# Optimization experiments

Hardware: AMD Instinct MI355X
Metric: run time of the kernel (lower is better)

Reference implementation:

```python
import jax, jax.numpy as jnp
import numpy as np

IMG, P, CIN, D, K, L, H, FF, B = 512, 32, 3, 256, 8192, 6, 8, 1024, 32
GRID = IMG // P  # 16
DH = D // H
EPS = 1e-5


def _ln(x, w, b):
    m = x.mean(-1, keepdims=True)
    v = ((x - m) ** 2).mean(-1, keepdims=True)
    return (x - m) / jnp.sqrt(v + EPS) * w + b


def _mha(x, wqkv, bqkv, wo, bo):
    # x: (S, Bt, D) -- axis 0 is the attention axis (torch batch_first=False quirk)
    S, Bt, _ = x.shape
    qkv = x @ wqkv.T + bqkv
    q, k, v = jnp.split(qkv, 3, axis=-1)
    q = q.reshape(S, Bt, H, DH)
    k = k.reshape(S, Bt, H, DH)
    v = v.reshape(S, Bt, H, DH)
    scores = jnp.einsum('sbhd,tbhd->bhst', q, k) / jnp.sqrt(jnp.float32(DH))
    attn = jax.nn.softmax(scores, axis=-1)
    o = jnp.einsum('bhst,tbhd->sbhd', attn, v).reshape(S, Bt, D)
    return o @ wo.T + bo


def _conv_t(x, w, b, stride=2, pad=1):
    # w uses torch ConvTranspose2d layout (Cin, Cout, kH, kW)
    kH = w.shape[2]
    wf = jnp.flip(w, (2, 3)).transpose(1, 0, 2, 3)  # -> (Cout, Cin, kH, kW)
    y = jax.lax.conv_general_dilated(
        x, wf, window_strides=(1, 1),
        padding=[(kH - 1 - pad, kH - 1 - pad)] * 2,
        lhs_dilation=(stride, stride),
        dimension_numbers=('NCHW', 'OIHW', 'NCHW'))
    return y + b[None, :, None, None]


def _forward(x, patch_w, patch_b, qkv_w, qkv_b, out_w, out_b, ln1_w, ln1_b,
             ln2_w, ln2_b, ff1_w, ff1_b, ff2_w, ff2_b, lnf_w, lnf_b, codebook,
             dec_w0, dec_b0, dec_w1, dec_b1, dec_w2, dec_b2, dec_w3, dec_b3):
    # patch embedding: conv stride=patch -> (B, D, G, G) -> (B, N, D)
    h = jax.lax.conv_general_dilated(
        x, patch_w, (P, P), 'VALID',
        dimension_numbers=('NCHW', 'OIHW', 'NCHW')) + patch_b[None, :, None, None]
    h = h.reshape(h.shape[0], D, -1).transpose(0, 2, 1)  # (B, N, D)
    # torch TransformerEncoderLayer default batch_first=False: attention runs
    # over axis 0 (image batch); faithfully replicated here. Post-norm, eval
    # mode (dropout=identity), exact gelu.
    for i in range(L):
        a = _mha(h, qkv_w[i], qkv_b[i], out_w[i], out_b[i])
        h = _ln(h + a, ln1_w[i], ln1_b[i])
        f = jax.nn.gelu(h @ ff1_w[i].T + ff1_b[i], approximate=False) @ ff2_w[i].T + ff2_b[i]
        h = _ln(h + f, ln2_w[i], ln2_b[i])
    h = _ln(h, lnf_w, lnf_b)
    # vector quantization: squared-distance argmin over codebook
    flat = h.reshape(-1, D)  # (B*N, D)
    d = ((flat ** 2).sum(-1, keepdims=True)
         - 2.0 * flat @ codebook.T
         + (codebook ** 2).sum(-1))  # (B*N, K)
    idx = jnp.argmin(d, axis=1)
    q = codebook[idx].reshape(h.shape)
    e_loss = jnp.mean((jax.lax.stop_gradient(q) - h) ** 2)
    q_loss = jnp.mean((q - jax.lax.stop_gradient(h)) ** 2)
    vq_loss = q_loss + 0.25 * e_loss
    q = h + jax.lax.stop_gradient(q - h)  # straight-through
    q = q.transpose(0, 2, 1).reshape(x.shape[0], D, GRID, GRID)
    y = jax.nn.relu(_conv_t(q, dec_w0, dec_b0))
    y = jax.nn.relu(_conv_t(y, dec_w1, dec_b1))
    y = jax.nn.relu(_conv_t(y, dec_w2, dec_b2))
    x_hat = jax.nn.sigmoid(_conv_t(y, dec_w3, dec_b3))
    return x_hat, vq_loss


def setup_inputs() -> dict:
    key = jax.random.key(0)
    ks = iter(jax.random.split(key, 64))
    nrm = lambda shape, s=0.02: jax.random.normal(next(ks), shape, jnp.float32) * s
    f32 = jnp.float32
    return {
        'x': jax.random.normal(next(ks), (B, CIN, IMG, IMG), f32),
        'patch_w': nrm((D, CIN, P, P)),
        'patch_b': jnp.zeros((D,), f32),
        'qkv_w': nrm((L, 3 * D, D)),
        'qkv_b': jnp.zeros((L, 3 * D), f32),
        'out_w': nrm((L, D, D)),
        'out_b': jnp.zeros((L, D), f32),
        'ln1_w': jnp.ones((L, D), f32),
        'ln1_b': jnp.zeros((L, D), f32),
        'ln2_w': jnp.ones((L, D), f32),
        'ln2_b': jnp.zeros((L, D), f32),
        'ff1_w': nrm((L, FF, D)),
        'ff1_b': jnp.zeros((L, FF), f32),
        'ff2_w': nrm((L, D, FF)),
        'ff2_b': jnp.zeros((L, D), f32),
        'lnf_w': jnp.ones((D,), f32),
        'lnf_b': jnp.zeros((D,), f32),
        'codebook': jax.random.uniform(next(ks), (K, D), f32, -1.0 / K, 1.0 / K),
        'dec_w0': nrm((D, 256, 4, 4)),
        'dec_b0': jnp.zeros((256,), f32),
        'dec_w1': nrm((256, 128, 4, 4)),
        'dec_b1': jnp.zeros((128,), f32),
        'dec_w2': nrm((128, 64, 4, 4)),
        'dec_b2': jnp.zeros((64,), f32),
        'dec_w3': nrm((64, CIN, 4, 4)),
        'dec_b3': jnp.zeros((CIN,), f32),
    }


def reference(x, patch_w, patch_b, qkv_w, qkv_b, out_w, out_b, ln1_w, ln1_b,
              ln2_w, ln2_b, ff1_w, ff1_b, ff2_w, ff2_b, lnf_w, lnf_b, codebook,
              dec_w0, dec_b0, dec_w1, dec_b1, dec_w2, dec_b2, dec_w3, dec_b3):
    return _forward(x, patch_w, patch_b, qkv_w, qkv_b, out_w, out_b, ln1_w,
                    ln1_b, ln2_w, ln2_b, ff1_w, ff1_b, ff2_w, ff2_b, lnf_w,
                    lnf_b, codebook, dec_w0, dec_b0, dec_w1, dec_b1, dec_w2,
                    dec_b2, dec_w3, dec_b3)
```

## Files before the change

### kernel.cpp

```cpp
#include <hip/hip_runtime.h>
#include <hip/hip_bf16.h>
#include <math.h>

typedef __hip_bfloat16 bf16;
typedef unsigned int u32;
typedef unsigned long long u64;
using short8 = __attribute__((ext_vector_type(8))) short;
using f32x4  = __attribute__((ext_vector_type(4))) float;

__device__ __forceinline__ float b2f(bf16 v){ return __bfloat162float(v); }
__device__ __forceinline__ bf16  f2b(float v){ return __float2bfloat16(v); }
__device__ __forceinline__ float plo(u32 u){ return __uint_as_float(u << 16); }
__device__ __forceinline__ float phi(u32 u){ return __uint_as_float(u & 0xffff0000u); }

__device__ __forceinline__ void gld16(const void* g, void* l)
{
  __builtin_amdgcn_global_load_lds(
      (const __attribute__((address_space(1))) u32*)g,
      (__attribute__((address_space(3))) u32*)l, 16, 0, 0);
}

__global__ void k_detect(const u32* probe, int* flag)
{
  if (threadIdx.x == 0 && blockIdx.x == 0)
    *flag = (*probe == 0x3F800000u) ? 0 : 1;
}

struct PPack { const void* s[25]; u32 off[26]; };
__global__ __launch_bounds__(256) void k_convall(PPack pp, bf16* P, const int* flag)
{
  const u32 i = blockIdx.x * 256 + threadIdx.x;
  if (i >= pp.off[25]) return;
  int lo = 0, hi = 25;
  while (hi - lo > 1) { const int mid = (lo + hi) >> 1; if (i >= pp.off[mid]) lo = mid; else hi = mid; }
  const u32 j = i - pp.off[lo];
  P[i] = *flag ? ((const bf16*)pp.s[lo])[j] : f2b(((const float*)pp.s[lo])[j]);
}

__global__ __launch_bounds__(256) void k_zero(u32* p, int n)
{
  const int i = blockIdx.x * 256 + threadIdx.x;
  if (i < n) p[i] = 0;
}

__global__ __launch_bounds__(128) void k_im2col(const void* x, bf16* A, const int* flag)
{
  const int m = blockIdx.y;
  const int k8 = blockIdx.x * 128 + threadIdx.x;
  const int k = k8 * 8;
  const int b = m >> 8, n = m & 255;
  const int gy = n >> 4, gx = n & 15;
  const int c = k >> 10, r = (k >> 5) & 31, pp = k & 31;
  const size_t src = (((size_t)(b * 3 + c) * 512) + gy * 32 + r) * 512 + gx * 32 + pp;
  bf16 ov[8];
  if (*flag) {
    const bf16* xp = (const bf16*)x + src;
    #pragma unroll
    for (int i = 0; i < 8; ++i) ov[i] = xp[i];
  } else {
    const float4 v0 = *reinterpret_cast<const float4*>((const float*)x + src);
    const float4 v1 = *reinterpret_cast<const float4*>((const float*)x + src + 4);
    ov[0]=f2b(v0.x); ov[1]=f2b(v0.y); ov[2]=f2b(v0.z); ov[3]=f2b(v0.w);
    ov[4]=f2b(v1.x); ov[5]=f2b(v1.y); ov[6]=f2b(v1.z); ov[7]=f2b(v1.w);
  }
  *reinterpret_cast<uint4*>(A + (size_t)m * 3072 + k) = *reinterpret_cast<const uint4*>(ov);
}

template<int EPI, int FM, bool DB>
__global__ __launch_bounds__(256, 2) void gemm_t(
    const bf16* __restrict__ A, const bf16* __restrict__ Bw,
    const bf16* __restrict__ bias, bf16* C, float* __restrict__ Cf,
    const float* __restrict__ cnorm, u64* __restrict__ ku,
    int M, int N, int K, int Kc)
{
  constexpr int BM = FM * 32;
  __shared__ alignas(16) bf16 As[DB ? 2 : 1][BM * 64];
  __shared__ alignas(16) bf16 Bs[DB ? 2 : 1][128 * 64];
  const int tid = threadIdx.x;
  const int bn = blockIdx.x * 128, bm = blockIdx.y * BM;
  const int z = blockIdx.z;
  const int kb = z * Kc;
  const int l = tid & 63, w = tid >> 6;
  const int wm = w >> 1, wn = w & 1;
  const int lg = l >> 4, lr = l & 15;
  const int sr8 = l >> 3;
  const int sch = (l & 7) ^ sr8;
  f32x4 acc[FM][4];
  #pragma unroll
  for (int fm = 0; fm < FM; ++fm)
    #pragma unroll
    for (int fn = 0; fn < 4; ++fn) acc[fm][fn] = (f32x4){0.f, 0.f, 0.f, 0.f};

  auto stage = [&](int bb, int k0) {
    char* ab = (char*)As[bb];
    char* bp = (char*)Bs[bb];
    #pragma unroll
    for (int it = 0; it < FM; ++it) {
      const int r = w * 8 + it * 32 + sr8;
      gld16(A + (size_t)(bm + r) * K + k0 + sch * 8, ab + w * 1024 + it * 4096);
    }
    #pragma unroll
    for (int it = 0; it < 4; ++it) {
      const int r = w * 8 + it * 32 + sr8;
      gld16(Bw + (size_t)(bn + r) * K + k0 + sch * 8, bp + w * 1024 + it * 4096);
    }
  };
  auto compute = [&](int bb) {
    const char* ab = (const char*)As[bb];
    const char* bp = (const char*)Bs[bb];
    #pragma unroll
    for (int ks = 0; ks < 2; ++ks) {
      short8 af[FM], bfr[4];
      #pragma unroll
      for (int fm = 0; fm < FM; ++fm) {
        const int r = wm * (FM * 16) + fm * 16 + lr;
        af[fm] = *reinterpret_cast<const short8*>(ab + r * 128 + (((lg + ks * 4) ^ (r & 7)) * 16));
      }
      #pragma unroll
      for (int fn = 0; fn < 4; ++fn) {
        const int r = wn * 64 + fn * 16 + lr;
        bfr[fn] = *reinterpret_cast<const short8*>(bp + r * 128 + (((lg + ks * 4) ^ (r & 7)) * 16));
      }
      #pragma unroll
      for (int fm = 0; fm < FM; ++fm)
        #pragma unroll
        for (int fn = 0; fn < 4; ++fn)
          acc[fm][fn] = __builtin_amdgcn_mfma_f32_16x16x32_bf16(af[fm], bfr[fn], acc[fm][fn], 0, 0, 0);
    }
  };

  const int nt = Kc >> 6;
  if (DB) {
    stage(0, kb);
    __syncthreads();
    for (int t = 0; t < nt; ++t) {
      const int cur = t & 1;
      if (t + 1 < nt) stage(cur ^ 1, kb + ((t + 1) << 6));
      compute(cur);
      __syncthreads();
    }
  } else {
    for (int t = 0; t < nt; ++t) {
      if (t) __syncthreads();
      stage(0, kb + (t << 6));
      __syncthreads();
      compute(0);
    }
  }

  if (EPI == 3) {
    __shared__ u64 skey[128][2];
    float cn4[4];
    #pragma unroll
    for (int fn = 0; fn < 4; ++fn) cn4[fn] = cnorm[bn + wn * 64 + fn * 16 + lr];
    #pragma unroll
    for (int fm = 0; fm < FM; ++fm) {
      #pragma unroll
      for (int r = 0; r < 4; ++r) {
        u64 best = ~0ull;
        #pragma unroll
        for (int fn = 0; fn < 4; ++fn) {
          const int col = bn + wn * 64 + fn * 16 + lr;
          const float d = cn4[fn] - 2.0f * acc[fm][fn][r];
          u32 u = __float_as_uint(d);
          u = (u & 0x80000000u) ? ~u : (u | 0x80000000u);
          const u64 key = ((u64)u << 32) | (u32)col;
          best = key < best ? key : best;
        }
        #pragma unroll
        for (int mk = 1; mk < 16; mk <<= 1) {
          const u64 o = __shfl_xor(best, mk, 64);
          best = o < best ? o : best;
        }
        if (lr == 0) skey[wm * 64 + fm * 16 + lg * 4 + r][wn] = best;
      }
    }
    __syncthreads();
    if (tid < 128) {
      const u64 a = skey[tid][0], b = skey[tid][1];
      ku[(size_t)blockIdx.x * M + bm + tid] = a < b ? a : b;
    }
  } else if (EPI == 4) {
    #pragma unroll
    for (int fm = 0; fm < FM; ++fm) {
      const int m0 = bm + wm * (FM * 16) + fm * 16 + lg * 4;
      #pragma unroll
      for (int fn = 0; fn < 4; ++fn) {
        const int n = bn + wn * 64 + fn * 16 + lr;
        #pragma unroll
        for (int r = 0; r < 4; ++r)
          Cf[((size_t)z * M + m0 + r) * N + n] = acc[fm][fn][r];
      }
    }
  } else {
    #pragma unroll
    for (int fm = 0; fm < FM; ++fm) {
      const int m0 = bm + wm * (FM * 16) + fm * 16 + lg * 4;
      #pragma unroll
      for (int fn = 0; fn < 4; ++fn) {
        const int n = bn + wn * 64 + fn * 16 + lr;
        const float bs = b2f(bias[n]);
        #pragma unroll
        for (int r = 0; r < 4; ++r) {
          float v = acc[fm][fn][r] + bs;
          if (EPI == 1) v = 0.5f * v * (1.0f + erff(v * 0.70710678118654752f));
          C[(size_t)(m0 + r) * N + n] = f2b(v);
        }
      }
    }
  }
}

template<bool DOLN>
__global__ __launch_bounds__(256) void k_lnred(
    const float* __restrict__ Pf, const bf16* __restrict__ bias,
    const bf16* res, const bf16* __restrict__ lw, const bf16* __restrict__ lb,
    bf16* h, int kc)
{
  __shared__ float red[256];
  __shared__ float stat[2];
  const int row = blockIdx.x, d = threadIdx.x;
  float s = 0.f;
  for (int z = 0; z < kc; ++z) s += Pf[((size_t)z * 8192 + row) * 256 + d];
  s += b2f(bias[d]);
  if (res) s += b2f(res[(size_t)row * 256 + d]);
  if (!DOLN) { h[(size_t)row * 256 + d] = f2b(s); return; }
  red[d] = s;
  __syncthreads();
  for (int off = 128; off > 0; off >>= 1) {
    if (d < off) red[d] += red[d + off];
    __syncthreads();
  }
  if (d == 0) stat[0] = red[0] * (1.0f / 256.0f);
  __syncthreads();
  const float m = stat[0];
  red[d] = (s - m) * (s - m);
  __syncthreads();
  for (int off = 128; off > 0; off >>= 1) {
    if (d < off) red[d] += red[d + off];
    __syncthreads();
  }
  if (d == 0) stat[1] = 1.0f / sqrtf(red[0] * (1.0f / 256.0f) + 1e-5f);
  __syncthreads();
  h[(size_t)row * 256 + d] = f2b((s - m) * stat[1] * b2f(lw[d]) + b2f(lb[d]));
}

__global__ __launch_bounds__(256) void k_vqmerge(
    const u64* __restrict__ ku, int* __restrict__ idx, int M, int NB)
{
  const int r = blockIdx.x * 256 + threadIdx.x;
  if (r >= M) return;
  u64 best = ku[r];
  for (int nb = 1; nb < NB; ++nb) {
    const u64 k = ku[(size_t)nb * M + r];
    best = k < best ? k : best;
  }
  idx[r] = (int)(best & 0xFFFFFFFFull);
}

__global__ __launch_bounds__(256) void k_cnorm(const bf16* __restrict__ cb, float* __restrict__ cn)
{
  const int j = blockIdx.x * 256 + threadIdx.x;
  const u32* p = (const u32*)(cb + (size_t)j * 256);
  float s = 0.f;
  for (int k = 0; k < 128; ++k) {
    const u32 v = p[k];
    const float a = plo(v), b = phi(v);
    s += a * a + b * b;
  }
  cn[j] = s;
}

__global__ __launch_bounds__(256) void k_ln(
    bf16* h, const bf16* w, const bf16* b)
{
  __shared__ float red[256];
  __shared__ float stat[2];
  const int row = blockIdx.x, d = threadIdx.x;
  const size_t base = (size_t)row * 256;
  const float x = b2f(h[base + d]);
  red[d] = x;
  __syncthreads();
  for (int off = 128; off > 0; off >>= 1) {
    if (d < off) red[d] += red[d + off];
    __syncthreads();
  }
  if (d == 0) stat[0] = red[0] * (1.0f / 256.0f);
  __syncthreads();
  const float m = stat[0];
  red[d] = (x - m) * (x - m);
  __syncthreads();
  for (int off = 128; off > 0; off >>= 1) {
    if (d < off) red[d] += red[d + off];
    __syncthreads();
  }
  if (d == 0) stat[1] = 1.0f / sqrtf(red[0] * (1.0f / 256.0f) + 1e-5f);
  __syncthreads();
  h[base + d] = f2b((x - m) * stat[1] * b2f(w[d]) + b2f(b[d]));
}

__global__ __launch_bounds__(256) void k_attn(
    const bf16* qkv, bf16* o)
{
  __shared__ float qs[32][33], ks[32][33], vs[32][33], ps[32][33];
  __shared__ float rs[32];
  const int bt = blockIdx.x, hd = blockIdx.y;
  const int tid = threadIdx.x;
  for (int e = 0; e < 4; ++e) {
    const int elem = tid + 256 * e;
    const int s = elem >> 5, c = elem & 31;
    const bf16* p = qkv + (size_t)(s * 256 + bt) * 768 + hd * 32 + c;
    qs[s][c] = b2f(p[0]);
    ks[s][c] = b2f(p[256]);
    vs[s][c] = b2f(p[512]);
  }
  __syncthreads();
  const int s = tid >> 3, j = tid & 7;
  float sc[4];
  #pragma unroll
  for (int e = 0; e < 4; ++e) {
    const int t = j + 8 * e;
    float v = 0.f;
    #pragma unroll
    for (int dd = 0; dd < 32; ++dd) v += qs[s][dd] * ks[t][dd];
    sc[e] = v * 0.17677669529663687f;
  }
  float mx = fmaxf(fmaxf(sc[0], sc[1]), fmaxf(sc[2], sc[3]));
  #pragma unroll
  for (int mk = 1; mk < 8; mk <<= 1) mx = fmaxf(mx, __shfl_xor(mx, mk, 64));
  float sm = 0.f; float ex[4];
  #pragma unroll
  for (int e = 0; e < 4; ++e) { ex[e] = expf(sc[e] - mx); sm += ex[e]; }
  #pragma unroll
  for (int mk = 1; mk < 8; mk <<= 1) sm += __shfl_xor(sm, mk, 64);
  #pragma unroll
  for (int e = 0; e < 4; ++e) ps[s][j + 8 * e] = ex[e];
  if (j == 0) rs[s] = 1.0f / sm;
  __syncthreads();
  #pragma unroll
  for (int e = 0; e < 4; ++e) {
    const int dd = j + 8 * e;
    float acc = 0.f;
    #pragma unroll
    for (int t = 0; t < 32; ++t) acc += ps[s][t] * vs[t][dd];
    o[(size_t)(s * 256 + bt) * 256 + hd * 32 + dd] = f2b(acc * rs[s]);
  }
}

__global__ __launch_bounds__(256) void k_gather(
    const bf16* h, const bf16* cb, const int* idx, bf16* a0, float* lsum)
{
  __shared__ float red[256];
  const int row = blockIdx.x, d = threadIdx.x;
  const int code = idx[row] & 8191;
  const float q = b2f(cb[(size_t)code * 256 + d]);
  const float x = b2f(h[(size_t)row * 256 + d]);
  red[d] = (q - x) * (q - x);
  __syncthreads();
  for (int off = 128; off > 0; off >>= 1) {
    if (d < off) red[d] += red[d + off];
    __syncthreads();
  }
  if (d == 0) lsum[row] = red[0];
  const int b = row >> 8, n = row & 255;
  const int y = n >> 4, xc = n & 15;
  a0[(((size_t)b * 18 + y + 1) * 18 + (xc + 1)) * 256 + d] = f2b(q);
}

__global__ __launch_bounds__(256) void k_loss(const float* lsum, float* out)
{
  __shared__ float red[256];
  const int tid = threadIdx.x;
  float v = 0.f;
  for (int i = 0; i < 32; ++i) v += lsum[tid + 256 * i];
  red[tid] = v;
  __syncthreads();
  for (int off = 128; off > 0; off >>= 1) {
    if (tid < off) red[tid] += red[tid + off];
    __syncthreads();
  }
  if (tid == 0)
    out[0] = red[0] * (1.25f / 2097152.0f);
}

__global__ __launch_bounds__(256) void k_wtrans(
    const bf16* __restrict__ w, bf16* __restrict__ wt,
    int Cin, int lCin, int CoutR, int CoutP)
{
  const int K = Cin << 2;
  const int total = 4 * CoutP * K;
  const int i = blockIdx.x * 256 + threadIdx.x;
  if (i >= total) return;
  const int p = i / (CoutP * K);
  const int rem = i - p * (CoutP * K);
  const int co = rem / K;
  const int k = rem - co * K;
  const int tap = k >> lCin, ci = k - (tap << lCin);
  const int py = p >> 1, px = p & 1, ty = tap >> 1, tx = tap & 1;
  bf16 v = f2b(0.f);
  if (co < CoutR)
    v = w[(((size_t)ci * CoutR + co) * 4 + py + 2 * ty) * 4 + px + 2 * tx];
  wt[i] = v;
}

__global__ __launch_bounds__(256, 2) void convt64(
    const bf16* __restrict__ in, const bf16* __restrict__ Wt,
    const bf16* __restrict__ bias, bf16* __restrict__ outp,
    int H, int lH, int Cin, int lCin, int Cout)
{
  __shared__ alignas(16) bf16 As[2][128 * 64];
  __shared__ alignas(16) bf16 Bs[2][64 * 64];
  const int tid = threadIdx.x;
  const int pz = blockIdx.z;
  const int py = pz >> 1, px = pz & 1;
  const int K = Cin << 2;
  const int bn = blockIdx.x * 64, bm = blockIdx.y * 128;
  const bf16* Bw = Wt + (size_t)pz * Cout * K;
  const int l = tid & 63, w = tid >> 6;
  const int wm = w >> 1, wn = w & 1;
  const int lg = l >> 4, lr = l & 15;
  const int sr8 = l >> 3;
  const int sch = (l & 7) ^ sr8;
  const int Hp = H + 2;
  f32x4 acc[4][2];
  #pragma unroll
  for (int fm = 0; fm < 4; ++fm)
    #pragma unroll
    for (int fn = 0; fn < 2; ++fn) acc[fm][fn] = (f32x4){0.f, 0.f, 0.f, 0.f};

  size_t pixbase[4];
  #pragma unroll
  for (int it = 0; it < 4; ++it) {
    const int m = bm + w * 8 + it * 32 + sr8;
    const int b = m >> (2 * lH);
    const int rem = m & ((1 << (2 * lH)) - 1);
    const int jj = rem >> lH, ii = rem & (H - 1);
    pixbase[it] = ((size_t)(b * Hp + jj) * Hp + ii);
  }

  auto stage = [&](int bb, int k0) {
    char* ab = (char*)As[bb];
    char* bp = (char*)Bs[bb];
    const int tap = k0 >> lCin;
    const int ty = tap >> 1, tx = tap & 1;
    const int sy = (1 - py) + (1 - ty);
    const int sx = (1 - px) + (1 - tx);
    const int ci0 = (k0 - (tap << lCin)) + sch * 8;
    #pragma unroll
    for (int it = 0; it < 4; ++it)
      gld16(in + (pixbase[it] + (size_t)sy * Hp + sx) * Cin + ci0,
            ab + w * 1024 + it * 4096);
    #pragma unroll
    for (int it = 0; it < 2; ++it) {
      const int r = w * 8 + it * 32 + sr8;
      gld16(Bw + (size_t)(bn + r) * K + k0 + sch * 8, bp + w * 1024 + it * 4096);
    }
  };

  const int nt = K >> 6;
  stage(0, 0);
  __syncthreads();
  for (int t = 0; t < nt; ++t) {
    const int cur = t & 1;
    if (t + 1 < nt) stage(cur ^ 1, (t + 1) << 6);
    const char* ab = (const char*)As[cur];
    const char* bb = (const char*)Bs[cur];
    #pragma unroll
    for (int ks = 0; ks < 2; ++ks) {
      short8 af[4], bfr[2];
      #pragma unroll
      for (int fm = 0; fm < 4; ++fm) {
        const int r = wm * 64 + fm * 16 + lr;
        af[fm] = *reinterpret_cast<const short8*>(ab + r * 128 + (((lg + ks * 4) ^ (r & 7)) * 16));
      }
      #pragma unroll
      for (int fn = 0; fn < 2; ++fn) {
        const int r = wn * 32 + fn * 16 + lr;
        bfr[fn] = *reinterpret_cast<const short8*>(bb + r * 128 + (((lg + ks * 4) ^ (r & 7)) * 16));
      }
      #pragma unroll
      for (int fm = 0; fm < 4; ++fm)
        #pragma unroll
        for (int fn = 0; fn < 2; ++fn)
          acc[fm][fn] = __builtin_amdgcn_mfma_f32_16x16x32_bf16(af[fm], bfr[fn], acc[fm][fn], 0, 0, 0);
    }
    __syncthreads();
  }

  const int Ho = 2 * H, Hop = Ho + 2;
  #pragma unroll
  for (int fm = 0; fm < 4; ++fm) {
    const int m0 = bm + wm * 64 + fm * 16 + lg * 4;
    #pragma unroll
    for (int fn = 0; fn < 2; ++fn) {
      const int n = bn + wn * 32 + fn * 16 + lr;
      #pragma unroll
      for (int r = 0; r < 4; ++r) {
        const int m = m0 + r;
        const int b = m >> (2 * lH);
        const int rem = m & ((1 << (2 * lH)) - 1);
        const int jj = rem >> lH, ii = rem & (H - 1);
        const int oy = 2 * jj + (1 - py), ox = 2 * ii + (1 - px);
        const float v = fmaxf(acc[fm][fn][r] + b2f(bias[n]), 0.f);
        outp[((size_t)(b * Hop + oy + 1) * Hop + ox + 1) * Cout + n] = f2b(v);
      }
    }
  }
}

__global__ __launch_bounds__(256) void k_dec3(
    const bf16* __restrict__ a3, const bf16* __restrict__ wt3,
    const bf16* __restrict__ bias, float* __restrict__ xhat, int chunkBase)
{
  __shared__ float wl[4][3][256];
  const int tid = threadIdx.x;
  for (int i = tid; i < 3072; i += 256) {
    const int pz = i / 768;
    const int rem = i - pz * 768;
    const int co = rem >> 8, k = rem & 255;
    wl[pz][co][k] = b2f(wt3[(pz * 3 + co) * 256 + k]);
  }
  __syncthreads();
  const int b = blockIdx.y;
  const int t = blockIdx.x;
  const int oy = (t >> 4) * 16 + (tid >> 4);
  const int ox = (t & 15) * 16 + (tid & 15);
  const int py = (oy + 1) & 1, px = (ox + 1) & 1;
  const int jj = (oy - 1 + py) >> 1, ii = (ox - 1 + px) >> 1;
  const int pz = py * 2 + px;
  float a0 = 0.f, a1 = 0.f, a2 = 0.f;
  #pragma unroll
  for (int ty = 0; ty < 2; ++ty) {
    #pragma unroll
    for (int tx = 0; tx < 2; ++tx) {
      const int sy = (1 - py) + (1 - ty), sx = (1 - px) + (1 - tx);
      const int tap = ty * 2 + tx;
      const u32* ip = (const u32*)(a3 + ((size_t)(b * 130 + jj + sy) * 130 + ii + sx) * 64);
      const float* w0 = &wl[pz][0][tap * 64];
      const float* w1 = &wl[pz][1][tap * 64];
      const float* w2 = &wl[pz][2][tap * 64];
      #pragma unroll
      for (int kk = 0; kk < 32; ++kk) {
        const u32 v = ip[kk];
        const float e0 = plo(v), e1 = phi(v);
        a0 += e0 * w0[2 * kk] + e1 * w0[2 * kk + 1];
        a1 += e0 * w1[2 * kk] + e1 * w1[2 * kk + 1];
        a2 += e0 * w2[2 * kk] + e1 * w2[2 * kk + 1];
      }
    }
  }
  const int n = chunkBase + b;
  const size_t ob = (size_t)n * 3 * 65536 + oy * 256 + ox;
  xhat[ob]           = 1.0f / (1.0f + expf(-(a0 + b2f(bias[0]))));
  xhat[ob + 65536]   = 1.0f / (1.0f + expf(-(a1 + b2f(bias[1]))));
  xhat[ob + 131072]  = 1.0f / (1.0f + expf(-(a2 + b2f(bias[2]))));
}

extern "C" void kernel_launch(void* const* d_in, const int* in_sizes, int n_in,
                              void* d_out, int out_size, void* d_ws, size_t ws_size,
                              hipStream_t stream)
{
  float* xhat = (float*)d_out;
  float* lossout = xhat + (out_size - 1);

  const size_t NEED = 130195456;
  if (ws_size < NEED) return;

  char* ws = (char*)d_ws;
  int*   flag  = (int*)  (ws + 0);
  float* lsum  = (float*)(ws + 1024);
  int*   idx   = (int*)  (ws + 65536);
  u64*   ku    = (u64*)  (ws + 131072);
  bf16*  P     = (bf16*) (ws + 8519680);
  bf16*  WT    = (bf16*) (ws + 27262976);
  float* cnorm = (float*)(ws + 30900224);
  bf16*  hbuf  = (bf16*) (ws + 31457280);
  bf16*  A_im  = (bf16*) (ws + 35651584);
  bf16*  qkvb  = (bf16*) (ws + 35651584);
  bf16*  obuf  = (bf16*) (ws + 48234496);
  bf16*  ffb   = (bf16*) (ws + 52428800);
  float* Pf    = (float*)(ws + 85983232);
  bf16*  a0    = (bf16*) (ws + 35651584);
  bf16*  a1    = (bf16*) (ws + 40960000);
  bf16*  a2    = (bf16*) (ws + 59899904);
  bf16*  a3    = (bf16*) (ws + 95584256);

  k_detect<<<1, 64, 0, stream>>>((const u32*)d_in[7], flag);

  size_t poff[26]; poff[1] = 0;
  for (int i = 2; i <= 25; ++i) poff[i] = poff[i - 1] + (size_t)in_sizes[i - 1];
  const size_t ptotal = poff[25] + (size_t)in_sizes[25];
  PPack pp;
  for (int i = 0; i < 25; ++i) { pp.s[i] = d_in[i + 1]; pp.off[i] = (u32)poff[i + 1]; }
  pp.off[25] = (u32)ptotal;
  k_convall<<<(int)((ptotal + 255) / 256), 256, 0, stream>>>(pp, P, flag);

  const bf16 *patch_w = P + poff[1],  *patch_b = P + poff[2];
  const bf16 *qkv_w   = P + poff[3],  *qkv_b   = P + poff[4];
  const bf16 *out_w   = P + poff[5],  *out_b   = P + poff[6];
  const bf16 *ln1_w   = P + poff[7],  *ln1_b   = P + poff[8];
  const bf16 *ln2_w   = P + poff[9],  *ln2_b   = P + poff[10];
  const bf16 *ff1_w   = P + poff[11], *ff1_b   = P + poff[12];
  const bf16 *ff2_w   = P + poff[13], *ff2_b   = P + poff[14];
  const bf16 *lnf_w   = P + poff[15], *lnf_b   = P + poff[16];
  const bf16 *codebook= P + poff[17];
  const bf16 *dec_w0  = P + poff[18], *dec_b0  = P + poff[19];
  const bf16 *dec_w1  = P + poff[20], *dec_b1  = P + poff[21];
  const bf16 *dec_w2  = P + poff[22], *dec_b2  = P + poff[23];
  const bf16 *dec_w3  = P + poff[24], *dec_b3  = P + poff[25];

  bf16* wt0 = WT;
  bf16* wt1 = wt0 + 1048576;
  bf16* wt2 = wt1 + 524288;
  bf16* wt3 = wt2 + 131072;
  k_wtrans<<<(1048576 + 255) / 256, 256, 0, stream>>>(dec_w0, wt0, 256, 8, 256, 256);
  k_wtrans<<<(524288 + 255) / 256, 256, 0, stream>>>(dec_w1, wt1, 256, 8, 128, 128);
  k_wtrans<<<(131072 + 255) / 256, 256, 0, stream>>>(dec_w2, wt2, 128, 7, 64, 64);
  k_wtrans<<<(3072 + 255) / 256, 256, 0, stream>>>(dec_w3, wt3, 64, 6, 3, 3);
  k_cnorm<<<32, 256, 0, stream>>>(codebook, cnorm);

  k_im2col<<<dim3(3, 8192), 128, 0, stream>>>(d_in[0], A_im, flag);
  gemm_t<4, 2, true><<<dim3(2, 128, 4), 256, 0, stream>>>(
      A_im, patch_w, nullptr, nullptr, Pf, nullptr, nullptr, 8192, 256, 3072, 768);
  k_lnred<false><<<8192, 256, 0, stream>>>(
      Pf, patch_b, nullptr, nullptr, nullptr, hbuf, 4);

  for (int l = 0; l < 6; ++l) {
    gemm_t<0, 2, false><<<dim3(6, 128, 1), 256, 0, stream>>>(
        hbuf, qkv_w + (size_t)l * 768 * 256, qkv_b + l * 768, qkvb, nullptr,
        nullptr, nullptr, 8192, 768, 256, 256);
    k_attn<<<dim3(256, 8), 256, 0, stream>>>(qkvb, obuf);
    gemm_t<4, 2, false><<<dim3(2, 128, 1), 256, 0, stream>>>(
        obuf, out_w + (size_t)l * 256 * 256, nullptr, nullptr, Pf,
        nullptr, nullptr, 8192, 256, 256, 256);
    k_lnred<true><<<8192, 256, 0, stream>>>(
        Pf, out_b + l * 256, hbuf, ln1_w + l * 256, ln1_b + l * 256, hbuf, 1);
    gemm_t<1, 2, false><<<dim3(8, 128, 1), 256, 0, stream>>>(
        hbuf, ff1_w + (size_t)l * 1024 * 256, ff1_b + l * 1024, ffb, nullptr,
        nullptr, nullptr, 8192, 1024, 256, 256);
    gemm_t<4, 2, false><<<dim3(2, 128, 4), 256, 0, stream>>>(
        ffb, ff2_w + (size_t)l * 256 * 1024, nullptr, nullptr, Pf,
        nullptr, nullptr, 8192, 256, 1024, 256);
    k_lnred<true><<<8192, 256, 0, stream>>>(
        Pf, ff2_b + l * 256, hbuf, ln2_w + l * 256, ln2_b + l * 256, hbuf, 4);
  }
  k_ln<<<8192, 256, 0, stream>>>(hbuf, lnf_w, lnf_b);

  gemm_t<3, 4, false><<<dim3(64, 64, 1), 256, 0, stream>>>(
      hbuf, codebook, nullptr, nullptr, nullptr, cnorm, ku, 8192, 8192, 256, 256);
  k_vqmerge<<<32, 256, 0, stream>>>(ku, idx, 8192, 64);

  k_zero<<<(1327104 + 255) / 256, 256, 0, stream>>>((u32*)a0, 1327104);
  k_gather<<<8192, 256, 0, stream>>>(hbuf, codebook, idx, a0, lsum);
  k_loss<<<1, 256, 0, stream>>>(lsum, lossout);

  k_zero<<<(4734976 + 255) / 256, 256, 0, stream>>>((u32*)a1, 4734976);
  k_zero<<<(8921088 + 255) / 256, 256, 0, stream>>>((u32*)a2, 8921088);
  k_zero<<<(8652800 + 255) / 256, 256, 0, stream>>>((u32*)a3, 8652800);

  convt64<<<dim3(4, 64, 4), 256, 0, stream>>>(a0, wt0, dec_b0, a1, 16, 4, 256, 8, 256);
  convt64<<<dim3(2, 256, 4), 256, 0, stream>>>(a1, wt1, dec_b1, a2, 32, 5, 256, 8, 128);
  for (int c = 0; c < 2; ++c) {
    const bf16* a2c = a2 + (size_t)c * 16 * 66 * 66 * 128;
    convt64<<<dim3(1, 512, 4), 256, 0, stream>>>(a2c, wt2, dec_b2, a3, 64, 6, 128, 7, 64);
    k_dec3<<<dim3(256, 16), 256, 0, stream>>>(a3, wt3, dec_b3, xhat, c * 16);
  }
}
```

Baseline: 1.116 ms.

## Split final deconv over parity blocks and 4-lane channel groups with shuffle reduction

```diff
diff --git a/kernel.cpp b/kernel.cpp
--- a/kernel.cpp
+++ b/kernel.cpp
@@ -512,22 +512,19 @@
     const bf16* __restrict__ a3, const bf16* __restrict__ wt3,
     const bf16* __restrict__ bias, float* __restrict__ xhat, int chunkBase)
 {
-  __shared__ float wl[4][3][256];
+  __shared__ float wl[3][264];
   const int tid = threadIdx.x;
-  for (int i = tid; i < 3072; i += 256) {
-    const int pz = i / 768;
-    const int rem = i - pz * 768;
-    const int co = rem >> 8, k = rem & 255;
-    wl[pz][co][k] = b2f(wt3[(pz * 3 + co) * 256 + k]);
-  }
-  __syncthreads();
-  const int b = blockIdx.y;
-  const int t = blockIdx.x;
-  const int oy = (t >> 4) * 16 + (tid >> 4);
-  const int ox = (t & 15) * 16 + (tid & 15);
-  const int py = (oy + 1) & 1, px = (ox + 1) & 1;
-  const int jj = (oy - 1 + py) >> 1, ii = (ox - 1 + px) >> 1;
-  const int pz = py * 2 + px;
+  const int pz = blockIdx.y;
+  const int py = pz >> 1, px = pz & 1;
+  for (int i = tid; i < 768; i += 256) {
+    const int co = i >> 8, k = i & 255;
+    wl[co][k] = b2f(wt3[(pz * 3 + co) * 256 + k]);
+  }
+  __syncthreads();
+  const int b = blockIdx.z;
+  const int p = blockIdx.x * 64 + (tid >> 2);
+  const int jj = p >> 7, ii = p & 127;
+  const int ch4 = tid & 3;
   float a0 = 0.f, a1 = 0.f, a2 = 0.f;
   #pragma unroll
   for (int ty = 0; ty < 2; ++ty) {
@@ -535,12 +532,12 @@
     for (int tx = 0; tx < 2; ++tx) {
       const int sy = (1 - py) + (1 - ty), sx = (1 - px) + (1 - tx);
       const int tap = ty * 2 + tx;
-      const u32* ip = (const u32*)(a3 + ((size_t)(b * 130 + jj + sy) * 130 + ii + sx) * 64);
-      const float* w0 = &wl[pz][0][tap * 64];
-      const float* w1 = &wl[pz][1][tap * 64];
-      const float* w2 = &wl[pz][2][tap * 64];
-      #pragma unroll
-      for (int kk = 0; kk < 32; ++kk) {
+      const u32* ip = (const u32*)(a3 + ((size_t)(b * 130 + jj + sy) * 130 + ii + sx) * 64) + ch4 * 8;
+      const float* w0 = &wl[0][tap * 64 + ch4 * 16];
+      const float* w1 = &wl[1][tap * 64 + ch4 * 16];
+      const float* w2 = &wl[2][tap * 64 + ch4 * 16];
+      #pragma unroll
+      for (int kk = 0; kk < 8; ++kk) {
         const u32 v = ip[kk];
         const float e0 = plo(v), e1 = phi(v);
         a0 += e0 * w0[2 * kk] + e1 * w0[2 * kk + 1];
@@ -549,11 +546,16 @@
       }
     }
   }
-  const int n = chunkBase + b;
-  const size_t ob = (size_t)n * 3 * 65536 + oy * 256 + ox;
-  xhat[ob]           = 1.0f / (1.0f + expf(-(a0 + b2f(bias[0]))));
-  xhat[ob + 65536]   = 1.0f / (1.0f + expf(-(a1 + b2f(bias[1]))));
-  xhat[ob + 131072]  = 1.0f / (1.0f + expf(-(a2 + b2f(bias[2]))));
+  a0 += __shfl_xor(a0, 1, 64); a0 += __shfl_xor(a0, 2, 64);
+  a1 += __shfl_xor(a1, 1, 64); a1 += __shfl_xor(a1, 2, 64);
+  a2 += __shfl_xor(a2, 1, 64); a2 += __shfl_xor(a2, 2, 64);
+  if (ch4 < 3) {
+    const float av = ch4 == 0 ? a0 : (ch4 == 1 ? a1 : a2);
+    const int oy = 2 * jj + (1 - py), ox = 2 * ii + (1 - px);
+    const float t = av + b2f(bias[ch4]);
+    xhat[(((size_t)(chunkBase + b) * 3 + ch4) * 256 + oy) * 256 + ox] =
+        1.0f / (1.0f + expf(-t));
+  }
 }
 
 extern "C" void kernel_launch(void* const* d_in, const int* in_sizes, int n_in,
@@ -663,6 +665,6 @@
   for (int c = 0; c < 2; ++c) {
     const bf16* a2c = a2 + (size_t)c * 16 * 66 * 66 * 128;
     convt64<<<dim3(1, 512, 4), 256, 0, stream>>>(a2c, wt2, dec_b2, a3, 64, 6, 128, 7, 64);
-    k_dec3<<<dim3(256, 16), 256, 0, stream>>>(a3, wt3, dec_b3, xhat, c * 16);
-  }
-}
+    k_dec3<<<dim3(256, 4, 16), 256, 0, stream>>>(a3, wt3, dec_b3, xhat, c * 16);
+  }
+}
```

Result: faster. 1.005 ms (-10.0%).
